# Kernel tuning notes

Measured on AMD Instinct MI355X. Metric: run time of the kernel, lower is better.

## Reference

```python
import jax, jax.numpy as jnp
import numpy as np

B, I, H = 32768, 512, 512


def _uniform(key, shape, fan_in):
    bound = 1.0 / np.sqrt(fan_in)
    return jax.random.uniform(key, shape, jnp.float32, -bound, bound)


def setup_inputs() -> dict:
    key = jax.random.key(0)
    ks = jax.random.split(key, 16)
    inp = {
        "x": jax.random.normal(ks[0], (B, I), jnp.float32),
        "h": jax.random.normal(ks[1], (B, H), jnp.float32),
        "c_prev": jax.random.normal(ks[2], (B, H), jnp.float32),
        # weights stored as [in, out] so we apply x @ W (transpose of torch layout)
        "Wxi": _uniform(ks[3], (I, H), I), "bxi": _uniform(ks[4], (H,), I),
        "Whi": _uniform(ks[5], (H, H), H),
        "Wxf": _uniform(ks[6], (I, H), I), "bxf": _uniform(ks[7], (H,), I),
        "Whf": _uniform(ks[8], (H, H), H),
        "Wxc": _uniform(ks[9], (I, H), I), "bxc": _uniform(ks[10], (H,), I),
        "Whc": _uniform(ks[11], (H, H), H),
        "Wxo": _uniform(ks[12], (I, H), I), "bxo": _uniform(ks[13], (H,), I),
        "Who": _uniform(ks[14], (H, H), H),
    }
    return inp


def reference(x, h, c_prev, Wxi, bxi, Whi, Wxf, bxf, Whf, Wxc, bxc, Whc, Wxo, bxo, Who):
    # Faithful to source: peephole (w_c) projections are dead code; the
    # forget path f*c_prev is computed then discarded, so c_next = i * tanh(.)
    i = jax.nn.sigmoid(x @ Wxi + bxi + h @ Whi)            # input gate
    f = jax.nn.sigmoid(x @ Wxf + bxf + h @ Whf)            # computed, unused (as in source)
    c_next = i * jnp.tanh(x @ Wxc + bxc + h @ Whc)         # NOTE: no f*c_prev term (source bug)
    o = jax.nn.sigmoid(x @ Wxo + bxo + h @ Who)            # output gate
    h_next = o * jnp.tanh(c_next)
    del f, c_prev  # unused, matching the original module's effective math
    return (h_next, c_next)
```

## Files before the change

kernel.cpp:

```cpp
#include <hip/hip_runtime.h>
#include <hip/hip_bf16.h>


typedef unsigned short u16;
typedef u16 u16x8 __attribute__((ext_vector_type(8)));
typedef __bf16 bf16x8 __attribute__((ext_vector_type(8)));
typedef float f32x4 __attribute__((ext_vector_type(4)));

#define B_DIM 32768
#define H_DIM 512
#define K_DIM 1024
#define BH_ELEMS (B_DIM * H_DIM)

__device__ __forceinline__ float bf2f(u16 u) {
    unsigned v = ((unsigned)u) << 16;
    float f;
    __builtin_memcpy(&f, &v, 4);
    return f;
}

__device__ __forceinline__ u16 f2bf16u(float f) {
    __hip_bfloat16 b = __float2bfloat16(f);
    u16 u;
    __builtin_memcpy(&u, &b, 2);
    return u;
}

__device__ __forceinline__ float fast_sigmoid(float x) {
    return 1.0f / (1.0f + __expf(-x));
}

__device__ __forceinline__ float fast_tanh(float x) {
    float e = __expf(-2.0f * fabsf(x));
    float r = (1.0f - e) / (1.0f + e);
    return x < 0.0f ? -r : r;
}

__global__ void probe_dtype(const unsigned* __restrict__ x, int* __restrict__ flag) {
    const int lane = threadIdx.x;
    const unsigned lo = x[lane] & 0xFFFFu;
    const unsigned e = (lo >> 7) & 0xFFu;
    const bool sane = (e >= 100u && e <= 140u) || (lo == 0u);
    const unsigned long long m = __ballot(sane);
    if (lane == 0) *flag = (__popcll(m) >= 48) ? 1 : 0;
}

__global__ void pack_weights(const void* __restrict__ Wxi, const void* __restrict__ Whi,
                             const void* __restrict__ Wxc, const void* __restrict__ Whc,
                             const void* __restrict__ Wxo, const void* __restrict__ Who,
                             const int* __restrict__ flag, u16* __restrict__ Wt)
{
    __shared__ u16 tile[32][33];
    const bool isbf = (*flag != 0);
    const int g = blockIdx.z >> 1, half = blockIdx.z & 1;
    const void* src;
    if (g == 0)      src = half ? Whi : Wxi;
    else if (g == 1) src = half ? Whc : Wxc;
    else             src = half ? Who : Wxo;
    const int kk = blockIdx.y * 32, nn = blockIdx.x * 32;
    const int tx = threadIdx.x, ty = threadIdx.y;
    if (isbf) {
        const u16* s = (const u16*)src;
#pragma unroll
        for (int i2 = 0; i2 < 4; ++i2)
            tile[ty + 8 * i2][tx] = s[(kk + ty + 8 * i2) * 512 + nn + tx];
    } else {
        const float* s = (const float*)src;
#pragma unroll
        for (int i2 = 0; i2 < 4; ++i2)
            tile[ty + 8 * i2][tx] = f2bf16u(s[(kk + ty + 8 * i2) * 512 + nn + tx]);
    }
    __syncthreads();
#pragma unroll
    for (int i2 = 0; i2 < 4; ++i2)
        Wt[(long)g * 524288 + (long)(nn + ty + 8 * i2) * 1024 + half * 512 + kk + tx]
            = tile[tx][ty + 8 * i2];
}

__global__ __launch_bounds__(256, 2) void lstm_gemm(
    const void* __restrict__ x, const void* __restrict__ h,
    const u16* __restrict__ Wt,
    const void* __restrict__ bxi, const void* __restrict__ bxc,
    const void* __restrict__ bxo, const int* __restrict__ flag,
    void* __restrict__ out)
{
    __shared__ __align__(16) u16 As[128 * 32];
    __shared__ __align__(16) u16 Bs[3 * 64 * 32];

    const bool isbf = (*flag != 0);
    const int tid    = threadIdx.x;
    const int lane   = tid & 63;
    const int wave   = tid >> 6;
    const int wave_m = wave & 1;
    const int wave_n = wave >> 1;
    const int m0 = blockIdx.y * 128;
    const int n0 = blockIdx.x * 64;

    const int trow = tid >> 2, tkc = (tid & 3) * 8;
    const long a_g0 = (long)(m0 + trow)      * 512 + tkc;
    const long a_g1 = (long)(m0 + 64 + trow) * 512 + tkc;
    const int  a_l0 = tid * 8;
    const int  a_l1 = 2048 + tid * 8;
    long b_g[3];
#pragma unroll
    for (int q = 0; q < 3; ++q)
        b_g[q] = (long)q * 524288 + (long)(n0 + trow) * 1024 + tkc;

    int a_ld[4];
#pragma unroll
    for (int mt = 0; mt < 4; ++mt)
        a_ld[mt] = (wave_m * 64 + mt * 16 + (lane & 15)) * 32 + (lane >> 4) * 8;
    int b_ld[3][2];
#pragma unroll
    for (int g = 0; g < 3; ++g)
#pragma unroll
        for (int nt = 0; nt < 2; ++nt)
            b_ld[g][nt] = g * 2048 + (wave_n * 32 + nt * 16 + (lane & 15)) * 32 + (lane >> 4) * 8;

    f32x4 acc[3][4][2];
    const f32x4 zero = {0.f, 0.f, 0.f, 0.f};
#pragma unroll
    for (int g = 0; g < 3; ++g)
#pragma unroll
        for (int mt = 0; mt < 4; ++mt)
#pragma unroll
            for (int nt = 0; nt < 2; ++nt)
                acc[g][mt][nt] = zero;

    for (int k0 = 0; k0 < K_DIM; k0 += 32) {
        const void* src = (k0 < 512) ? x : h;
        const long kadj = (k0 < 512) ? k0 : (k0 - 512);

        bf16x8 av0, av1, bv[3];
        if (isbf) {
            const u16* s = (const u16*)src + kadj;
            u16x8 t0 = *(const u16x8*)(s + a_g0);
            u16x8 t1 = *(const u16x8*)(s + a_g1);
            __builtin_memcpy(&av0, &t0, 16);
            __builtin_memcpy(&av1, &t1, 16);
        } else {
            const float* s = (const float*)src + kadj;
            f32x4 p0 = *(const f32x4*)(s + a_g0);
            f32x4 p1 = *(const f32x4*)(s + a_g0 + 4);
            f32x4 q0 = *(const f32x4*)(s + a_g1);
            f32x4 q1 = *(const f32x4*)(s + a_g1 + 4);
#pragma unroll
            for (int j = 0; j < 4; ++j) {
                av0[j] = (__bf16)p0[j]; av0[4 + j] = (__bf16)p1[j];
                av1[j] = (__bf16)q0[j]; av1[4 + j] = (__bf16)q1[j];
            }
        }
#pragma unroll
        for (int q = 0; q < 3; ++q) {
            u16x8 t = *(const u16x8*)(Wt + b_g[q] + k0);
            __builtin_memcpy(&bv[q], &t, 16);
        }

        __syncthreads();
        *(bf16x8*)&As[a_l0] = av0;
        *(bf16x8*)&As[a_l1] = av1;
#pragma unroll
        for (int q = 0; q < 3; ++q)
            *(bf16x8*)&Bs[q * 2048 + tid * 8] = bv[q];
        __syncthreads();

        bf16x8 af[4];
#pragma unroll
        for (int mt = 0; mt < 4; ++mt)
            af[mt] = *(const bf16x8*)&As[a_ld[mt]];
        bf16x8 bfr[3][2];
#pragma unroll
        for (int g = 0; g < 3; ++g)
#pragma unroll
            for (int nt = 0; nt < 2; ++nt)
                bfr[g][nt] = *(const bf16x8*)&Bs[b_ld[g][nt]];

#pragma unroll
        for (int g = 0; g < 3; ++g)
#pragma unroll
            for (int mt = 0; mt < 4; ++mt)
#pragma unroll
            for (int nt = 0; nt < 2; ++nt)
                acc[g][mt][nt] = __builtin_amdgcn_mfma_f32_16x16x32_bf16(
                    af[mt], bfr[g][nt], acc[g][mt][nt], 0, 0, 0);
    }

    const int colbase = n0 + wave_n * 32 + (lane & 15);
    float bi[2], bc[2], bo[2];
#pragma unroll
    for (int nt = 0; nt < 2; ++nt) {
        const int col = colbase + nt * 16;
        if (isbf) {
            bi[nt] = bf2f(((const u16*)bxi)[col]);
            bc[nt] = bf2f(((const u16*)bxc)[col]);
            bo[nt] = bf2f(((const u16*)bxo)[col]);
        } else {
            bi[nt] = ((const float*)bxi)[col];
            bc[nt] = ((const float*)bxc)[col];
            bo[nt] = ((const float*)bxo)[col];
        }
    }

    const int rowbase = m0 + wave_m * 64 + (lane >> 4) * 4;
#pragma unroll
    for (int mt = 0; mt < 4; ++mt)
#pragma unroll
        for (int nt = 0; nt < 2; ++nt)
#pragma unroll
            for (int r = 0; r < 4; ++r) {
                const int row = rowbase + mt * 16 + r;
                const int col = colbase + nt * 16;
                const float iv = fast_sigmoid(acc[0][mt][nt][r] + bi[nt]);
                const float cv = iv * fast_tanh(acc[1][mt][nt][r] + bc[nt]);
                const float ov = fast_sigmoid(acc[2][mt][nt][r] + bo[nt]);
                const float hv = ov * fast_tanh(cv);
                const long idx = (long)row * 512 + col;
                if (isbf) {
                    ((u16*)out)[idx]            = f2bf16u(hv);
                    ((u16*)out)[BH_ELEMS + idx] = f2bf16u(cv);
                } else {
                    ((float*)out)[idx]            = hv;
                    ((float*)out)[BH_ELEMS + idx] = cv;
                }
            }
}

extern "C" void kernel_launch(void* const* d_in, const int* in_sizes, int n_in,
                              void* d_out, int out_size, void* d_ws, size_t ws_size,
                              hipStream_t stream) {
    const void* x   = d_in[0];
    const void* h   = d_in[1];
    const void* Wxi = d_in[3];
    const void* bxi = d_in[4];
    const void* Whi = d_in[5];
    const void* Wxc = d_in[9];
    const void* bxc = d_in[10];
    const void* Whc = d_in[11];
    const void* Wxo = d_in[12];
    const void* bxo = d_in[13];
    const void* Who = d_in[14];

    int* flag = (int*)d_ws;
    u16* Wt   = (u16*)((char*)d_ws + 256);

    probe_dtype<<<1, 64, 0, stream>>>((const unsigned*)x, flag);
    pack_weights<<<dim3(16, 16, 6), dim3(32, 8), 0, stream>>>(
        Wxi, Whi, Wxc, Whc, Wxo, Who, flag, Wt);
    lstm_gemm<<<dim3(8, 256), dim3(256), 0, stream>>>(
        x, h, Wt, bxi, bxc, bxo, flag, d_out);
}
```

Baseline: 454.8 us.

## Pre-convert activations to bf16 and stage tiles via global_load_lds with XOR swizzle

Adds a pre-pass that converts x and h to one contiguous bf16 buffer in workspace. The GEMM then loads A and B tiles straight into LDS with async global_load_lds and an XOR-swizzled layout, meant to cut LDS bank conflicts. This removes the per-tile fp32 loads, in-register conversion and register staging, and drops the dtype probe. The cost is an extra pass over 128 MB of activations and a 64 MB intermediate, and the bf16 input path no longer exists. A fallback kernel runs when the workspace is too small.

```diff
diff --git a/kernel.cpp b/kernel.cpp
--- a/kernel.cpp
+++ b/kernel.cpp
@@ -3,20 +3,17 @@
 
 
 typedef unsigned short u16;
-typedef u16 u16x8 __attribute__((ext_vector_type(8)));
 typedef __bf16 bf16x8 __attribute__((ext_vector_type(8)));
 typedef float f32x4 __attribute__((ext_vector_type(4)));
 
 #define B_DIM 32768
-#define H_DIM 512
 #define K_DIM 1024
-#define BH_ELEMS (B_DIM * H_DIM)
-
-__device__ __forceinline__ float bf2f(u16 u) {
-    unsigned v = ((unsigned)u) << 16;
-    float f;
-    __builtin_memcpy(&f, &v, 4);
-    return f;
+#define BH_ELEMS (B_DIM * 512)
+
+__device__ __forceinline__ void async_load16(const void* g, void* l) {
+    __builtin_amdgcn_global_load_lds(
+        (const __attribute__((address_space(1))) void*)g,
+        (__attribute__((address_space(3))) void*)l, 16, 0, 0);
 }
 
 __device__ __forceinline__ u16 f2bf16u(float f) {
@@ -36,40 +33,41 @@
     return x < 0.0f ? -r : r;
 }
 
-__global__ void probe_dtype(const unsigned* __restrict__ x, int* __restrict__ flag) {
-    const int lane = threadIdx.x;
-    const unsigned lo = x[lane] & 0xFFFFu;
-    const unsigned e = (lo >> 7) & 0xFFu;
-    const bool sane = (e >= 100u && e <= 140u) || (lo == 0u);
-    const unsigned long long m = __ballot(sane);
-    if (lane == 0) *flag = (__popcll(m) >= 48) ? 1 : 0;
-}
-
-__global__ void pack_weights(const void* __restrict__ Wxi, const void* __restrict__ Whi,
-                             const void* __restrict__ Wxc, const void* __restrict__ Whc,
-                             const void* __restrict__ Wxo, const void* __restrict__ Who,
-                             const int* __restrict__ flag, u16* __restrict__ Wt)
+__global__ void convert_u(const float* __restrict__ x, const float* __restrict__ h,
+                          __bf16* __restrict__ U)
+{
+    const int c = blockIdx.x * 256 + threadIdx.x;
+    const int row = c >> 6, cc = c & 63;
+    const float* xs = x + (long)row * 512 + cc * 8;
+    const float* hs = h + (long)row * 512 + cc * 8;
+    f32x4 a0 = *(const f32x4*)xs, a1 = *(const f32x4*)(xs + 4);
+    f32x4 b0 = *(const f32x4*)hs, b1 = *(const f32x4*)(hs + 4);
+    bf16x8 va, vb;
+#pragma unroll
+    for (int j = 0; j < 4; ++j) {
+        va[j] = (__bf16)a0[j]; va[4 + j] = (__bf16)a1[j];
+        vb[j] = (__bf16)b0[j]; vb[4 + j] = (__bf16)b1[j];
+    }
+    *(bf16x8*)(U + (long)row * 1024 + cc * 8)       = va;
+    *(bf16x8*)(U + (long)row * 1024 + 512 + cc * 8) = vb;
+}
+
+__global__ void pack_weights(const float* __restrict__ Wxi, const float* __restrict__ Whi,
+                             const float* __restrict__ Wxc, const float* __restrict__ Whc,
+                             const float* __restrict__ Wxo, const float* __restrict__ Who,
+                             u16* __restrict__ Wt)
 {
     __shared__ u16 tile[32][33];
-    const bool isbf = (*flag != 0);
     const int g = blockIdx.z >> 1, half = blockIdx.z & 1;
-    const void* src;
+    const float* src;
     if (g == 0)      src = half ? Whi : Wxi;
     else if (g == 1) src = half ? Whc : Wxc;
     else             src = half ? Who : Wxo;
     const int kk = blockIdx.y * 32, nn = blockIdx.x * 32;
     const int tx = threadIdx.x, ty = threadIdx.y;
-    if (isbf) {
-        const u16* s = (const u16*)src;
-#pragma unroll
-        for (int i2 = 0; i2 < 4; ++i2)
-            tile[ty + 8 * i2][tx] = s[(kk + ty + 8 * i2) * 512 + nn + tx];
-    } else {
-        const float* s = (const float*)src;
-#pragma unroll
-        for (int i2 = 0; i2 < 4; ++i2)
-            tile[ty + 8 * i2][tx] = f2bf16u(s[(kk + ty + 8 * i2) * 512 + nn + tx]);
-    }
+#pragma unroll
+    for (int i2 = 0; i2 < 4; ++i2)
+        tile[ty + 8 * i2][tx] = f2bf16u(src[(kk + ty + 8 * i2) * 512 + nn + tx]);
     __syncthreads();
 #pragma unroll
     for (int i2 = 0; i2 < 4; ++i2)
@@ -77,17 +75,14 @@
             = tile[tx][ty + 8 * i2];
 }
 
-__global__ __launch_bounds__(256, 2) void lstm_gemm(
-    const void* __restrict__ x, const void* __restrict__ h,
-    const u16* __restrict__ Wt,
-    const void* __restrict__ bxi, const void* __restrict__ bxc,
-    const void* __restrict__ bxo, const int* __restrict__ flag,
-    void* __restrict__ out)
+__global__ __launch_bounds__(256) void lstm_gemm_fast(
+    const u16* __restrict__ U, const u16* __restrict__ Wt,
+    const float* __restrict__ bxi, const float* __restrict__ bxc,
+    const float* __restrict__ bxo, float* __restrict__ out)
 {
     __shared__ __align__(16) u16 As[128 * 32];
     __shared__ __align__(16) u16 Bs[3 * 64 * 32];
 
-    const bool isbf = (*flag != 0);
     const int tid    = threadIdx.x;
     const int lane   = tid & 63;
     const int wave   = tid >> 6;
@@ -96,26 +91,35 @@
     const int m0 = blockIdx.y * 128;
     const int n0 = blockIdx.x * 64;
 
-    const int trow = tid >> 2, tkc = (tid & 3) * 8;
-    const long a_g0 = (long)(m0 + trow)      * 512 + tkc;
-    const long a_g1 = (long)(m0 + 64 + trow) * 512 + tkc;
-    const int  a_l0 = tid * 8;
-    const int  a_l1 = 2048 + tid * 8;
-    long b_g[3];
-#pragma unroll
-    for (int q = 0; q < 3; ++q)
-        b_g[q] = (long)q * 524288 + (long)(n0 + trow) * 1024 + tkc;
-
+    const int arow = tid >> 2;
+    const int kcl  = tid & 3;
+    const int kcg  = kcl ^ ((arow >> 1) & 3);
+    const long aoff0 = (long)(m0 + arow) * 1024 + kcg * 8;
+    const long aoff1 = aoff0 + (long)64 * 1024;
+    long boff[3];
+#pragma unroll
+    for (int j = 0; j < 3; ++j)
+        boff[j] = (long)j * 524288 + (long)(n0 + arow) * 1024 + kcg * 8;
+
+    u16* const aldst0 = &As[wave * 512];
+    u16* const aldst1 = &As[2048 + wave * 512];
+    u16* bldst[3];
+#pragma unroll
+    for (int j = 0; j < 3; ++j)
+        bldst[j] = &Bs[j * 2048 + wave * 512];
+
+    const int r15 = lane & 15, kc = lane >> 4;
+    const int key = kc ^ ((r15 >> 1) & 3);
     int a_ld[4];
 #pragma unroll
     for (int mt = 0; mt < 4; ++mt)
-        a_ld[mt] = (wave_m * 64 + mt * 16 + (lane & 15)) * 32 + (lane >> 4) * 8;
+        a_ld[mt] = ((wave_m * 64 + mt * 16 + r15) * 4 + key) * 8;
     int b_ld[3][2];
 #pragma unroll
     for (int g = 0; g < 3; ++g)
 #pragma unroll
         for (int nt = 0; nt < 2; ++nt)
-            b_ld[g][nt] = g * 2048 + (wave_n * 32 + nt * 16 + (lane & 15)) * 32 + (lane >> 4) * 8;
+            b_ld[g][nt] = g * 2048 + ((wave_n * 32 + nt * 16 + r15) * 4 + key) * 8;
 
     f32x4 acc[3][4][2];
     const f32x4 zero = {0.f, 0.f, 0.f, 0.f};
@@ -128,40 +132,12 @@
                 acc[g][mt][nt] = zero;
 
     for (int k0 = 0; k0 < K_DIM; k0 += 32) {
-        const void* src = (k0 < 512) ? x : h;
-        const long kadj = (k0 < 512) ? k0 : (k0 - 512);
-
-        bf16x8 av0, av1, bv[3];
-        if (isbf) {
-            const u16* s = (const u16*)src + kadj;
-            u16x8 t0 = *(const u16x8*)(s + a_g0);
-            u16x8 t1 = *(const u16x8*)(s + a_g1);
-            __builtin_memcpy(&av0, &t0, 16);
-            __builtin_memcpy(&av1, &t1, 16);
-        } else {
-            const float* s = (const float*)src + kadj;
-            f32x4 p0 = *(const f32x4*)(s + a_g0);
-            f32x4 p1 = *(const f32x4*)(s + a_g0 + 4);
-            f32x4 q0 = *(const f32x4*)(s + a_g1);
-            f32x4 q1 = *(const f32x4*)(s + a_g1 + 4);
-#pragma unroll
-            for (int j = 0; j < 4; ++j) {
-                av0[j] = (__bf16)p0[j]; av0[4 + j] = (__bf16)p1[j];
-                av1[j] = (__bf16)q0[j]; av1[4 + j] = (__bf16)q1[j];
-            }
-        }
-#pragma unroll
-        for (int q = 0; q < 3; ++q) {
-            u16x8 t = *(const u16x8*)(Wt + b_g[q] + k0);
-            __builtin_memcpy(&bv[q], &t, 16);
-        }
-
         __syncthreads();
-        *(bf16x8*)&As[a_l0] = av0;
-        *(bf16x8*)&As[a_l1] = av1;
-#pragma unroll
-        for (int q = 0; q < 3; ++q)
-            *(bf16x8*)&Bs[q * 2048 + tid * 8] = bv[q];
+        async_load16(U + aoff0 + k0, aldst0);
+        async_load16(U + aoff1 + k0, aldst1);
+#pragma unroll
+        for (int j = 0; j < 3; ++j)
+            async_load16(Wt + boff[j] + k0, bldst[j]);
         __syncthreads();
 
         bf16x8 af[4];
@@ -185,23 +161,14 @@
                     af[mt], bfr[g][nt], acc[g][mt][nt], 0, 0, 0);
     }
 
-    const int colbase = n0 + wave_n * 32 + (lane & 15);
+    const int colbase = n0 + wave_n * 32 + r15;
     float bi[2], bc[2], bo[2];
 #pragma unroll
     for (int nt = 0; nt < 2; ++nt) {
         const int col = colbase + nt * 16;
-        if (isbf) {
-            bi[nt] = bf2f(((const u16*)bxi)[col]);
-            bc[nt] = bf2f(((const u16*)bxc)[col]);
-            bo[nt] = bf2f(((const u16*)bxo)[col]);
-        } else {
-            bi[nt] = ((const float*)bxi)[col];
-            bc[nt] = ((const float*)bxc)[col];
-            bo[nt] = ((const float*)bxo)[col];
-        }
-    }
-
-    const int rowbase = m0 + wave_m * 64 + (lane >> 4) * 4;
+        bi[nt] = bxi[col]; bc[nt] = bxc[col]; bo[nt] = bxo[col];
+    }
+    const int rowbase = m0 + wave_m * 64 + kc * 4;
 #pragma unroll
     for (int mt = 0; mt < 4; ++mt)
 #pragma unroll
@@ -215,37 +182,144 @@
                 const float ov = fast_sigmoid(acc[2][mt][nt][r] + bo[nt]);
                 const float hv = ov * fast_tanh(cv);
                 const long idx = (long)row * 512 + col;
-                if (isbf) {
-                    ((u16*)out)[idx]            = f2bf16u(hv);
-                    ((u16*)out)[BH_ELEMS + idx] = f2bf16u(cv);
-                } else {
-                    ((float*)out)[idx]            = hv;
-                    ((float*)out)[BH_ELEMS + idx] = cv;
-                }
+                out[idx]            = hv;
+                out[BH_ELEMS + idx] = cv;
+            }
+}
+
+typedef u16 u16x8 __attribute__((ext_vector_type(8)));
+__global__ __launch_bounds__(256, 2) void lstm_gemm_fb(
+    const float* __restrict__ x, const float* __restrict__ h,
+    const u16* __restrict__ Wt,
+    const float* __restrict__ bxi, const float* __restrict__ bxc,
+    const float* __restrict__ bxo, float* __restrict__ out)
+{
+    __shared__ __align__(16) u16 As[128 * 32];
+    __shared__ __align__(16) u16 Bs[3 * 64 * 32];
+    const int tid = threadIdx.x, lane = tid & 63, wave = tid >> 6;
+    const int wave_m = wave & 1, wave_n = wave >> 1;
+    const int m0 = blockIdx.y * 128, n0 = blockIdx.x * 64;
+    const int trow = tid >> 2, tkc = (tid & 3) * 8;
+    const long a_g0 = (long)(m0 + trow) * 512 + tkc;
+    const long a_g1 = (long)(m0 + 64 + trow) * 512 + tkc;
+    long b_g[3];
+#pragma unroll
+    for (int q = 0; q < 3; ++q)
+        b_g[q] = (long)q * 524288 + (long)(n0 + trow) * 1024 + tkc;
+    int a_ld[4];
+#pragma unroll
+    for (int mt = 0; mt < 4; ++mt)
+        a_ld[mt] = (wave_m * 64 + mt * 16 + (lane & 15)) * 32 + (lane >> 4) * 8;
+    int b_ld[3][2];
+#pragma unroll
+    for (int g = 0; g < 3; ++g)
+#pragma unroll
+        for (int nt = 0; nt < 2; ++nt)
+            b_ld[g][nt] = g * 2048 + (wave_n * 32 + nt * 16 + (lane & 15)) * 32 + (lane >> 4) * 8;
+    f32x4 acc[3][4][2];
+    const f32x4 zero = {0.f, 0.f, 0.f, 0.f};
+#pragma unroll
+    for (int g = 0; g < 3; ++g)
+#pragma unroll
+        for (int mt = 0; mt < 4; ++mt)
+#pragma unroll
+            for (int nt = 0; nt < 2; ++nt) acc[g][mt][nt] = zero;
+    for (int k0 = 0; k0 < K_DIM; k0 += 32) {
+        const float* s = ((k0 < 512) ? x : h) + ((k0 < 512) ? k0 : (k0 - 512));
+        bf16x8 av0, av1, bv[3];
+        f32x4 p0 = *(const f32x4*)(s + a_g0), p1 = *(const f32x4*)(s + a_g0 + 4);
+        f32x4 q0 = *(const f32x4*)(s + a_g1), q1 = *(const f32x4*)(s + a_g1 + 4);
+#pragma unroll
+        for (int j = 0; j < 4; ++j) {
+            av0[j] = (__bf16)p0[j]; av0[4 + j] = (__bf16)p1[j];
+            av1[j] = (__bf16)q0[j]; av1[4 + j] = (__bf16)q1[j];
+        }
+#pragma unroll
+        for (int q = 0; q < 3; ++q) {
+            u16x8 t = *(const u16x8*)(Wt + b_g[q] + k0);
+            __builtin_memcpy(&bv[q], &t, 16);
+        }
+        __syncthreads();
+        *(bf16x8*)&As[tid * 8] = av0;
+        *(bf16x8*)&As[2048 + tid * 8] = av1;
+#pragma unroll
+        for (int q = 0; q < 3; ++q) *(bf16x8*)&Bs[q * 2048 + tid * 8] = bv[q];
+        __syncthreads();
+        bf16x8 af[4];
+#pragma unroll
+        for (int mt = 0; mt < 4; ++mt) af[mt] = *(const bf16x8*)&As[a_ld[mt]];
+        bf16x8 bfr[3][2];
+#pragma unroll
+        for (int g = 0; g < 3; ++g)
+#pragma unroll
+            for (int nt = 0; nt < 2; ++nt) bfr[g][nt] = *(const bf16x8*)&Bs[b_ld[g][nt]];
+#pragma unroll
+        for (int g = 0; g < 3; ++g)
+#pragma unroll
+            for (int mt = 0; mt < 4; ++mt)
+#pragma unroll
+            for (int nt = 0; nt < 2; ++nt)
+                acc[g][mt][nt] = __builtin_amdgcn_mfma_f32_16x16x32_bf16(
+                    af[mt], bfr[g][nt], acc[g][mt][nt], 0, 0, 0);
+    }
+    const int colbase = n0 + wave_n * 32 + (lane & 15);
+    float bi[2], bc[2], bo[2];
+#pragma unroll
+    for (int nt = 0; nt < 2; ++nt) {
+        const int col = colbase + nt * 16;
+        bi[nt] = bxi[col]; bc[nt] = bxc[col]; bo[nt] = bxo[col];
+    }
+    const int rowbase = m0 + wave_m * 64 + (lane >> 4) * 4;
+#pragma unroll
+    for (int mt = 0; mt < 4; ++mt)
+#pragma unroll
+        for (int nt = 0; nt < 2; ++nt)
+#pragma unroll
+            for (int r = 0; r < 4; ++r) {
+                const int row = rowbase + mt * 16 + r;
+                const int col = colbase + nt * 16;
+                const float iv = fast_sigmoid(acc[0][mt][nt][r] + bi[nt]);
+                const float cv = iv * fast_tanh(acc[1][mt][nt][r] + bc[nt]);
+                const float ov = fast_sigmoid(acc[2][mt][nt][r] + bo[nt]);
+                const float hv = ov * fast_tanh(cv);
+                const long idx = (long)row * 512 + col;
+                out[idx] = hv;
+                out[BH_ELEMS + idx] = cv;
             }
 }
 
 extern "C" void kernel_launch(void* const* d_in, const int* in_sizes, int n_in,
                               void* d_out, int out_size, void* d_ws, size_t ws_size,
                               hipStream_t stream) {
-    const void* x   = d_in[0];
-    const void* h   = d_in[1];
-    const void* Wxi = d_in[3];
-    const void* bxi = d_in[4];
-    const void* Whi = d_in[5];
-    const void* Wxc = d_in[9];
-    const void* bxc = d_in[10];
-    const void* Whc = d_in[11];
-    const void* Wxo = d_in[12];
-    const void* bxo = d_in[13];
-    const void* Who = d_in[14];
-
-    int* flag = (int*)d_ws;
-    u16* Wt   = (u16*)((char*)d_ws + 256);
-
-    probe_dtype<<<1, 64, 0, stream>>>((const unsigned*)x, flag);
-    pack_weights<<<dim3(16, 16, 6), dim3(32, 8), 0, stream>>>(
-        Wxi, Whi, Wxc, Whc, Wxo, Who, flag, Wt);
-    lstm_gemm<<<dim3(8, 256), dim3(256), 0, stream>>>(
-        x, h, Wt, bxi, bxc, bxo, flag, d_out);
-}
+    const float* x   = (const float*)d_in[0];
+    const float* h   = (const float*)d_in[1];
+    const float* Wxi = (const float*)d_in[3];
+    const float* bxi = (const float*)d_in[4];
+    const float* Whi = (const float*)d_in[5];
+    const float* Wxc = (const float*)d_in[9];
+    const float* bxc = (const float*)d_in[10];
+    const float* Whc = (const float*)d_in[11];
+    const float* Wxo = (const float*)d_in[12];
+    const float* bxo = (const float*)d_in[13];
+    const float* Who = (const float*)d_in[14];
+    float* out = (float*)d_out;
+
+    const size_t U_BYTES = (size_t)B_DIM * K_DIM * 2;
+    const size_t WT_BYTES = (size_t)3 * 512 * 1024 * 2;
+
+    if (ws_size >= U_BYTES + WT_BYTES) {
+        __bf16* U = (__bf16*)d_ws;
+        u16* Wt = (u16*)((char*)d_ws + U_BYTES);
+        convert_u<<<8192, 256, 0, stream>>>(x, h, U);
+        pack_weights<<<dim3(16, 16, 6), dim3(32, 8), 0, stream>>>(
+            Wxi, Whi, Wxc, Whc, Wxo, Who, Wt);
+        lstm_gemm_fast<<<dim3(8, 256), dim3(256), 0, stream>>>(
+            (const u16*)U, Wt, bxi, bxc, bxo, out);
+    } else {
+        u16* Wt = (u16*)d_ws;
+        pack_weights<<<dim3(16, 16, 6), dim3(32, 8), 0, stream>>>(
+            Wxi, Whi, Wxc, Whc, Wxo, Who, Wt);
+        lstm_gemm_fb<<<dim3(8, 256), dim3(256), 0, stream>>>(
+            x, h, Wt, bxi, bxc, bxo, out);
+    }
+}
```

Measured after the change: 545.3 us. +19.9%, slower.
